# Optimization experiments

Hardware: AMD Instinct MI355X
Metric: run time of the kernel (lower is better)

The kernel has to match this reference:

```python
import jax, jax.numpy as jnp
import numpy as np

IN_F = 4096
OUT_F = 4096
M_PAD = 4096   # next pow2 >= OUT_F
N_PAD = 4096   # next pow2 >= IN_F
CB_SIZE = 256  # E8 codebook entries, each an 8-dim vector


def fht(x):
    """Normalized fast Hadamard transform along the last axis (power-of-2 length)."""
    n = x.shape[-1]
    lead = x.shape[:-1]
    x = x.reshape(-1, n)
    h = 1
    while h < n:  # log2(n) static iterations -> jit-friendly
        x = x.reshape(-1, n // (2 * h), 2, h)
        a, b = x[:, :, 0, :], x[:, :, 1, :]
        x = jnp.stack((a + b, a - b), axis=2).reshape(-1, n)
        h *= 2
    return (x * np.float32(1.0 / np.sqrt(n))).reshape(*lead, n)


def setup_inputs() -> dict:
    key = jax.random.key(0)
    k_x, k_q, k_su, k_sv, k_cb = jax.random.split(key, 5)
    x = jax.random.normal(k_x, (4, 2048, IN_F), dtype=jnp.float32)
    Qidxs = jax.random.randint(k_q, (M_PAD, N_PAD // 8), 0, CB_SIZE, dtype=jnp.int32)
    # sign vectors are +-1 (random Hadamard transform signs)
    SU = jnp.where(jax.random.normal(k_su, (M_PAD,)) >= 0, 1.0, -1.0).astype(jnp.float32)
    SV = jnp.where(jax.random.normal(k_sv, (N_PAD,)) >= 0, 1.0, -1.0).astype(jnp.float32)
    Wscale = jnp.ones((), dtype=jnp.float32)
    codebook = jax.random.normal(k_cb, (CB_SIZE, 8), dtype=jnp.float32)
    return {"x": x, "Qidxs": Qidxs, "SU": SU, "SV": SV, "Wscale": Wscale, "codebook": codebook}


def reference(x, Qidxs, SU, SV, Wscale, codebook):
    shape = x.shape
    xf = x.reshape(-1, IN_F).astype(jnp.float32)          # (B, in)
    x_pad = jnp.pad(xf, ((0, 0), (0, N_PAD - IN_F)))      # (B, n_pad)
    # 1) input -> RHT domain: sign flip then Hadamard
    x_rht = fht(x_pad * SV[None, :])
    # 2) decode codebook indices into dense RHT-domain weight (m_pad, n_pad)
    W_rht = codebook[Qidxs.reshape(-1)].reshape(M_PAD, N_PAD)
    # 3) GEMM in RHT domain with global scale
    y_rht = (x_rht @ W_rht.T) * Wscale
    # 4) output RHT inverse: Hadamard then sign flip, unpad
    y = fht(y_rht) * SU[None, :]
    y = y[:, :OUT_F]
    return y.reshape(*shape[:-1], OUT_F)
```

## Files before the change

### kernel.cpp

```cpp
#include <hip/hip_runtime.h>
#include <hip/hip_bf16.h>


using short8 = __attribute__((ext_vector_type(8))) short;
using f32x4  = __attribute__((ext_vector_type(4))) float;

#define AS1 __attribute__((address_space(1)))
#define AS3 __attribute__((address_space(3)))

__device__ __forceinline__ unsigned short f2bf(float f) {
  unsigned int u = __float_as_uint(f);
  unsigned int r = (u + 0x7fffu + ((u >> 16) & 1u)) >> 16;
  return (unsigned short)r;
}

__device__ __forceinline__ void gload16(const void* g, void* l) {
  __builtin_amdgcn_global_load_lds((const AS1 void*)g, (AS3 void*)l, 16, 0, 0);
}

#define WAIT_VM4 asm volatile("s_waitcnt vmcnt(4)" ::: "memory")
#define WAIT_VM0 asm volatile("s_waitcnt vmcnt(0)" ::: "memory")
#define LGKM0    asm volatile("s_waitcnt lgkmcnt(0)" ::: "memory")
#define SB       __builtin_amdgcn_sched_barrier(0)
#define BAR      __builtin_amdgcn_s_barrier()
#define PRIO1    __builtin_amdgcn_s_setprio(1)
#define PRIO0    __builtin_amdgcn_s_setprio(0)

__global__ __launch_bounds__(256) void rht_in_kernel(const float* __restrict__ X,
                                                     const float* __restrict__ SV,
                                                     unsigned short* __restrict__ A) {
  __shared__ float tmp[4096];
  const int row = blockIdx.x;
  const int t = threadIdx.x;
  const size_t base = (size_t)row * 4096;
  float v[16];
#pragma unroll
  for (int j = 0; j < 16; ++j) {
    int c = j * 256 + t;
    v[j] = X[base + c] * SV[c];
  }
#pragma unroll
  for (int d = 1; d < 16; d <<= 1) {
#pragma unroll
    for (int j = 0; j < 16; ++j) {
      if ((j & d) == 0) {
        float a = v[j], b = v[j | d];
        v[j] = a + b;
        v[j | d] = a - b;
      }
    }
  }
  const int lane = t & 63;
#pragma unroll
  for (int d = 1; d < 64; d <<= 1) {
#pragma unroll
    for (int j = 0; j < 16; ++j) {
      float p = __shfl_xor(v[j], d, 64);
      v[j] = (lane & d) ? (p - v[j]) : (v[j] + p);
    }
  }
#pragma unroll
  for (int dd = 0; dd < 2; ++dd) {
    const int d = 64 << dd;
    if (dd) __syncthreads();
#pragma unroll
    for (int j = 0; j < 16; ++j) tmp[j * 256 + t] = v[j];
    __syncthreads();
#pragma unroll
    for (int j = 0; j < 16; ++j) {
      float p = tmp[j * 256 + (t ^ d)];
      v[j] = (t & d) ? (p - v[j]) : (v[j] + p);
    }
  }
#pragma unroll
  for (int j = 0; j < 16; ++j) A[base + j * 256 + t] = f2bf(v[j]);
}

__global__ __launch_bounds__(256) void decode_w_kernel(const int* __restrict__ Q,
                                                       const float* __restrict__ cb,
                                                       unsigned short* __restrict__ W) {
  const int e = blockIdx.x * 256 + threadIdx.x;
  const int idx = Q[e];
  const float4* c = (const float4*)(cb + (size_t)idx * 8);
  float4 c0 = c[0], c1 = c[1];
  union { short8 v; unsigned short u[8]; } w;
  w.u[0] = f2bf(c0.x); w.u[1] = f2bf(c0.y); w.u[2] = f2bf(c0.z); w.u[3] = f2bf(c0.w);
  w.u[4] = f2bf(c1.x); w.u[5] = f2bf(c1.y); w.u[6] = f2bf(c1.z); w.u[7] = f2bf(c1.w);
  *(short8*)&W[(size_t)e * 8] = w.v;
}

#define MFMA1(mi, ni, av, bv) \
  acc[mi][ni] = __builtin_amdgcn_mfma_f32_16x16x32_bf16(av, bv, acc[mi][ni], 0, 0, 0)

#define MFMA16(MB, a0_, a1_, a2_, a3_, bx0, bx1, bx2, bx3) do {           \
  MFMA1(MB + 0, 0, a0_, bx0); MFMA1(MB + 0, 1, a0_, bx1);                 \
  MFMA1(MB + 0, 2, a0_, bx2); MFMA1(MB + 0, 3, a0_, bx3);                 \
  MFMA1(MB + 1, 0, a1_, bx0); MFMA1(MB + 1, 1, a1_, bx1);                 \
  MFMA1(MB + 1, 2, a1_, bx2); MFMA1(MB + 1, 3, a1_, bx3);                 \
  MFMA1(MB + 2, 0, a2_, bx0); MFMA1(MB + 2, 1, a2_, bx1);                 \
  MFMA1(MB + 2, 2, a2_, bx2); MFMA1(MB + 2, 3, a2_, bx3);                 \
  MFMA1(MB + 3, 0, a3_, bx0); MFMA1(MB + 3, 1, a3_, bx1);                 \
  MFMA1(MB + 3, 2, a3_, bx2); MFMA1(MB + 3, 3, a3_, bx3);                 \
} while (0)

#define RD_A4(r0, r1, r2, r3, BC, KS, MB) do {                            \
  r0 = *(const short8*)&sA[BC][KS][wm + (MB + 0) * 16 + fr][qc];          \
  r1 = *(const short8*)&sA[BC][KS][wm + (MB + 1) * 16 + fr][qc];          \
  r2 = *(const short8*)&sA[BC][KS][wm + (MB + 2) * 16 + fr][qc];          \
  r3 = *(const short8*)&sA[BC][KS][wm + (MB + 3) * 16 + fr][qc];          \
} while (0)

#define RD_B4(r0, r1, r2, r3, BC, KS) do {                                \
  r0 = *(const short8*)&sB[BC][KS][wn + 0 * 16 + fr][qc];                 \
  r1 = *(const short8*)&sB[BC][KS][wn + 1 * 16 + fr][qc];                 \
  r2 = *(const short8*)&sB[BC][KS][wn + 2 * 16 + fr][qc];                 \
  r3 = *(const short8*)&sB[BC][KS][wn + 3 * 16 + fr][qc];                 \
} while (0)

#define STAGE_A(BB, H, KTN) do {                                          \
  const unsigned short* gp_ = Ag + (KTN) * 64 + (H) * 32;                 \
  gload16(gp_, (unsigned short*)&sA[BB][H][0][0] + d0);                   \
  gload16(gp_ + (size_t)128 * 4096, (unsigned short*)&sA[BB][H][0][0] + d1); \
} while (0)

#define STAGE_B(BB, H, KTN) do {                                          \
  const unsigned short* gp_ = Bg + (KTN) * 64 + (H) * 32;                 \
  gload16(gp_, (unsigned short*)&sB[BB][H][0][0] + d0);                   \
  gload16(gp_ + (size_t)128 * 4096, (unsigned short*)&sB[BB][H][0][0] + d1); \
} while (0)

#define TILE(BC, BN_, KTN, DS, LASTF) do {                                \
           \
  RD_A4(aS0_0, aS0_1, aS0_2, aS0_3, BC, 0, 0);                            \
  RD_B4(bA_0, bA_1, bA_2, bA_3, BC, 0);                                   \
  if (DS) { STAGE_A(BN_, 0, KTN); }                                       \
  BAR; LGKM0; SB;                                                         \
  RD_A4(aS1_0, aS1_1, aS1_2, aS1_3, BC, 0, 4); SB;                        \
  PRIO1; MFMA16(0, aS0_0, aS0_1, aS0_2, aS0_3, bA_0, bA_1, bA_2, bA_3);   \
  PRIO0; BAR;                                                             \
                 \
  if (DS) { STAGE_B(BN_, 0, KTN); }                                       \
  BAR; LGKM0; SB;                                                         \
  if (LASTF) { WAIT_VM0; } else { WAIT_VM4; }                             \
  RD_A4(aS0_0, aS0_1, aS0_2, aS0_3, BC, 1, 0);                            \
  RD_B4(bB_0, bB_1, bB_2, bB_3, BC, 1); SB;                               \
  PRIO1; MFMA16(4, aS1_0, aS1_1, aS1_2, aS1_3, bA_0, bA_1, bA_2, bA_3);   \
  PRIO0; BAR;                                                             \
                                     \
  if (DS) { STAGE_A(BN_, 1, KTN); }                                       \
  BAR; LGKM0; SB;                                                         \
  RD_A4(aS1_0, aS1_1, aS1_2, aS1_3, BC, 1, 4); SB;                        \
  PRIO1; MFMA16(0, aS0_0, aS0_1, aS0_2, aS0_3, bB_0, bB_1, bB_2, bB_3);   \
  PRIO0; BAR;                                                             \
            \
  if (DS) { STAGE_B(BN_, 1, KTN); }                                       \
  BAR; LGKM0; SB;                                                         \
  PRIO1; MFMA16(4, aS1_0, aS1_1, aS1_2, aS1_3, bB_0, bB_1, bB_2, bB_3);   \
  PRIO0;                                                                  \
  if (!(LASTF)) { WAIT_VM4; }                                             \
  BAR;                                                                    \
} while (0)

__global__ __launch_bounds__(512, 2) void gemm_bt_kernel(const unsigned short* __restrict__ A,
                                                         const unsigned short* __restrict__ B,
                                                         float* __restrict__ C) {
  __shared__ unsigned short sA[2][2][256][32];
  __shared__ unsigned short sB[2][2][256][32];

  const int bid = blockIdx.x;
  const int swz = (bid & 7) * 64 + (bid >> 3);
  const int tm = swz >> 4;
  const int tn = swz & 15;

  const int t = threadIdx.x;
  const int lane = t & 63;
  const int w = t >> 6;
  const int wm = (w >> 2) * 128;
  const int wn = (w & 3) * 64;
  const int fr = lane & 15;
  const int qc = ((lane >> 4) ^ ((lane >> 1) & 3)) * 8;

  const int sr = t >> 2;
  const int sc = ((t & 3) ^ ((t >> 3) & 3)) * 8;
  const unsigned short* Ag = A + (size_t)(tm * 256 + sr) * 4096 + sc;
  const unsigned short* Bg = B + (size_t)(tn * 256 + sr) * 4096 + sc;
  const int d0 = t * 8;
  const int d1 = (512 + t) * 8;

  f32x4 acc[8][4];
#pragma unroll
  for (int m = 0; m < 8; ++m)
#pragma unroll
    for (int n = 0; n < 4; ++n) {
      f32x4 z = {0.f, 0.f, 0.f, 0.f};
      acc[m][n] = z;
    }
  short8 aS0_0, aS0_1, aS0_2, aS0_3;
  short8 aS1_0, aS1_1, aS1_2, aS1_3;
  short8 bA_0, bA_1, bA_2, bA_3;
  short8 bB_0, bB_1, bB_2, bB_3;

  STAGE_A(0, 0, 0); STAGE_B(0, 0, 0); STAGE_A(0, 1, 0); STAGE_B(0, 1, 0);
  WAIT_VM4;
  BAR;

  for (int k2 = 0; k2 < 31; ++k2) {
    TILE(0, 1, 2 * k2 + 1, 1, 0);
    TILE(1, 0, 2 * k2 + 2, 1, 0);
  }
  TILE(0, 1, 63, 1, 0);
  TILE(1, 0, 64, 0, 1);

  const size_t crow0 = (size_t)tm * 256 + wm + (lane >> 4) * 4;
  const int ccol0 = tn * 256 + wn + fr;
#pragma unroll
  for (int mf = 0; mf < 8; ++mf)
#pragma unroll
    for (int j = 0; j < 4; ++j) {
      float* Cp = C + (crow0 + mf * 16 + j) * 4096 + ccol0;
#pragma unroll
      for (int nf = 0; nf < 4; ++nf) Cp[nf * 16] = acc[mf][nf][j];
    }
}

__global__ __launch_bounds__(256) void rht_out_kernel(float* __restrict__ Y,
                                                      const float* __restrict__ SU,
                                                      const float* __restrict__ Wscale) {
  __shared__ float tmp[4096];
  const int row = blockIdx.x;
  const int t = threadIdx.x;
  const size_t base = (size_t)row * 4096;
  float v[16];
#pragma unroll
  for (int j = 0; j < 16; ++j) v[j] = Y[base + j * 256 + t];
#pragma unroll
  for (int d = 1; d < 16; d <<= 1) {
#pragma unroll
    for (int j = 0; j < 16; ++j) {
      if ((j & d) == 0) {
        float a = v[j], b = v[j | d];
        v[j] = a + b;
        v[j | d] = a - b;
      }
    }
  }
  const int lane = t & 63;
#pragma unroll
  for (int d = 1; d < 64; d <<= 1) {
#pragma unroll
    for (int j = 0; j < 16; ++j) {
      float p = __shfl_xor(v[j], d, 64);
      v[j] = (lane & d) ? (p - v[j]) : (v[j] + p);
    }
  }
#pragma unroll
  for (int dd = 0; dd < 2; ++dd) {
    const int d = 64 << dd;
    if (dd) __syncthreads();
#pragma unroll
    for (int j = 0; j < 16; ++j) tmp[j * 256 + t] = v[j];
    __syncthreads();
#pragma unroll
    for (int j = 0; j < 16; ++j) {
      float p = tmp[j * 256 + (t ^ d)];
      v[j] = (t & d) ? (p - v[j]) : (v[j] + p);
    }
  }
  const float ws = Wscale[0] * (1.0f / 4096.0f);
#pragma unroll
  for (int j = 0; j < 16; ++j) {
    int c = j * 256 + t;
    Y[base + c] = v[j] * SU[c] * ws;
  }
}

extern "C" void kernel_launch(void* const* d_in, const int* in_sizes, int n_in,
                              void* d_out, int out_size, void* d_ws, size_t ws_size,
                              hipStream_t stream) {
  const float* x      = (const float*)d_in[0];
  const int*   Qidxs  = (const int*)d_in[1];
  const float* SU     = (const float*)d_in[2];
  const float* SV     = (const float*)d_in[3];
  const float* Wscale = (const float*)d_in[4];
  const float* cb     = (const float*)d_in[5];
  float* out = (float*)d_out;

  unsigned short* Arht = (unsigned short*)d_ws;
  unsigned short* W    = (unsigned short*)((char*)d_ws + (size_t)8192 * 4096 * 2);

  rht_in_kernel<<<8192, 256, 0, stream>>>(x, SV, Arht);
  decode_w_kernel<<<(4096 * 512) / 256, 256, 0, stream>>>(Qidxs, cb, W);
  gemm_bt_kernel<<<512, 512, 0, stream>>>(Arht, W, out);
  rht_out_kernel<<<8192, 256, 0, stream>>>(out, SU, Wscale);
}
```

Measured before the change: 356.3 us.

## Fold both Hadamard transforms into the decoded weight matrix

Because the Hadamard transforms are linear, they are applied to the 4096x4096 weight instead of to the 8192-row activations and outputs: W' = diag(SU)·H·W·H. The weight is decoded and row-transformed in one kernel, then column-transformed in two passes over bf16 intermediates. The GEMM then writes the final output directly, which removes the FHT over the input and output activations. The cost is extra bf16 rounding of the transformed weight at each pass, plus three weight passes over 4096x4096, with strided loads in the column passes.

```diff
diff --git a/kernel.cpp b/kernel.cpp
--- a/kernel.cpp
+++ b/kernel.cpp
@@ -12,6 +12,10 @@
   unsigned int u = __float_as_uint(f);
   unsigned int r = (u + 0x7fffu + ((u >> 16) & 1u)) >> 16;
   return (unsigned short)r;
+}
+
+__device__ __forceinline__ float bf2f(unsigned short u) {
+  return __uint_as_float((unsigned int)u << 16);
 }
 
 __device__ __forceinline__ void gload16(const void* g, void* l) {
@@ -26,37 +30,67 @@
 #define PRIO1    __builtin_amdgcn_s_setprio(1)
 #define PRIO0    __builtin_amdgcn_s_setprio(0)
 
-__global__ __launch_bounds__(256) void rht_in_kernel(const float* __restrict__ X,
-                                                     const float* __restrict__ SV,
-                                                     unsigned short* __restrict__ A) {
+#define H16_REGS(v)                                                       \
+  _Pragma("unroll")                                                       \
+  for (int d = 1; d < 16; d <<= 1) {                                      \
+    _Pragma("unroll")                                                     \
+    for (int j = 0; j < 16; ++j) {                                        \
+      if ((j & d) == 0) {                                                 \
+        float a_ = v[j], b_ = v[j | d];                                   \
+        v[j] = a_ + b_;                                                   \
+        v[j | d] = a_ - b_;                                               \
+      }                                                                   \
+    }                                                                     \
+  }
+
+__global__ __launch_bounds__(256) void zconv_kernel(const float* __restrict__ X,
+                                                    const float* __restrict__ SV,
+                                                    unsigned short* __restrict__ Z) {
+  const size_t idx = ((size_t)blockIdx.x * 256 + threadIdx.x) * 16;
+  const int c0 = (int)(idx & 4095);
+  const float4* X4 = (const float4*)(X + idx);
+  const float4* SV4 = (const float4*)(SV + c0);
+  union { short8 s; unsigned short u[8]; } lo, hi;
+#pragma unroll
+  for (int q = 0; q < 2; ++q) {
+    float4 a = X4[2 * q], b = X4[2 * q + 1];
+    float4 sa = SV4[2 * q], sb = SV4[2 * q + 1];
+    unsigned short* o = q ? hi.u : lo.u;
+    o[0] = f2bf(a.x * sa.x); o[1] = f2bf(a.y * sa.y);
+    o[2] = f2bf(a.z * sa.z); o[3] = f2bf(a.w * sa.w);
+    o[4] = f2bf(b.x * sb.x); o[5] = f2bf(b.y * sb.y);
+    o[6] = f2bf(b.z * sb.z); o[7] = f2bf(b.w * sb.w);
+  }
+  short8* Zp = (short8*)(Z + idx);
+  Zp[0] = lo.s;
+  Zp[1] = hi.s;
+}
+
+__global__ __launch_bounds__(256) void decode_rowfht_kernel(const int* __restrict__ Q,
+                                                            const float* __restrict__ cb,
+                                                            unsigned short* __restrict__ Wa) {
   __shared__ float tmp[4096];
   const int row = blockIdx.x;
   const int t = threadIdx.x;
-  const size_t base = (size_t)row * 4096;
+  const int lane = t & 63;
   float v[16];
-#pragma unroll
-  for (int j = 0; j < 16; ++j) {
-    int c = j * 256 + t;
-    v[j] = X[base + c] * SV[c];
-  }
-#pragma unroll
-  for (int d = 1; d < 16; d <<= 1) {
-#pragma unroll
-    for (int j = 0; j < 16; ++j) {
-      if ((j & d) == 0) {
-        float a = v[j], b = v[j | d];
-        v[j] = a + b;
-        v[j | d] = a - b;
-      }
-    }
-  }
-  const int lane = t & 63;
+  int2 qi = *(const int2*)&Q[(size_t)row * 512 + 2 * t];
+  {
+    const float4* c0 = (const float4*)(cb + (size_t)qi.x * 8);
+    const float4* c1 = (const float4*)(cb + (size_t)qi.y * 8);
+    float4 p0 = c0[0], p1 = c0[1], p2 = c1[0], p3 = c1[1];
+    v[0] = p0.x;  v[1] = p0.y;  v[2] = p0.z;  v[3] = p0.w;
+    v[4] = p1.x;  v[5] = p1.y;  v[6] = p1.z;  v[7] = p1.w;
+    v[8] = p2.x;  v[9] = p2.y;  v[10] = p2.z; v[11] = p2.w;
+    v[12] = p3.x; v[13] = p3.y; v[14] = p3.z; v[15] = p3.w;
+  }
+  H16_REGS(v)
 #pragma unroll
   for (int d = 1; d < 64; d <<= 1) {
 #pragma unroll
     for (int j = 0; j < 16; ++j) {
-      float p = __shfl_xor(v[j], d, 64);
-      v[j] = (lane & d) ? (p - v[j]) : (v[j] + p);
+      float p_ = __shfl_xor(v[j], d, 64);
+      v[j] = (lane & d) ? (p_ - v[j]) : (v[j] + p_);
     }
   }
 #pragma unroll
@@ -68,25 +102,69 @@
     __syncthreads();
 #pragma unroll
     for (int j = 0; j < 16; ++j) {
-      float p = tmp[j * 256 + (t ^ d)];
-      v[j] = (t & d) ? (p - v[j]) : (v[j] + p);
-    }
-  }
-#pragma unroll
-  for (int j = 0; j < 16; ++j) A[base + j * 256 + t] = f2bf(v[j]);
-}
-
-__global__ __launch_bounds__(256) void decode_w_kernel(const int* __restrict__ Q,
-                                                       const float* __restrict__ cb,
-                                                       unsigned short* __restrict__ W) {
-  const int e = blockIdx.x * 256 + threadIdx.x;
-  const int idx = Q[e];
-  const float4* c = (const float4*)(cb + (size_t)idx * 8);
-  float4 c0 = c[0], c1 = c[1];
-  union { short8 v; unsigned short u[8]; } w;
-  w.u[0] = f2bf(c0.x); w.u[1] = f2bf(c0.y); w.u[2] = f2bf(c0.z); w.u[3] = f2bf(c0.w);
-  w.u[4] = f2bf(c1.x); w.u[5] = f2bf(c1.y); w.u[6] = f2bf(c1.z); w.u[7] = f2bf(c1.w);
-  *(short8*)&W[(size_t)e * 8] = w.v;
+      float p_ = tmp[j * 256 + (t ^ d)];
+      v[j] = (t & d) ? (p_ - v[j]) : (v[j] + p_);
+    }
+  }
+  union { short8 s; unsigned short u[8]; } lo, hi;
+#pragma unroll
+  for (int j = 0; j < 8; ++j) {
+    lo.u[j] = f2bf(v[j] * (1.0f / 64.0f));
+    hi.u[j] = f2bf(v[8 + j] * (1.0f / 64.0f));
+  }
+  short8* Wp = (short8*)(Wa + (size_t)row * 4096 + t * 16);
+  Wp[0] = lo.s;
+  Wp[1] = hi.s;
+}
+
+template <int PASS>
+__global__ __launch_bounds__(256) void fht_wcol_kernel(const unsigned short* __restrict__ Win,
+                                                       unsigned short* __restrict__ Wout,
+                                                       const float* __restrict__ SU,
+                                                       const float* __restrict__ Wscale) {
+  __shared__ float tmp[64 * 64];
+  const int rg = blockIdx.x >> 6;
+  const int cg = blockIdx.x & 63;
+  const int t = threadIdx.x;
+  const int cl = t & 63;
+  const int q = t >> 6;
+  const int c = cg * 64 + cl;
+  float v[16];
+#pragma unroll
+  for (int j = 0; j < 16; ++j) {
+    const int rloc = q * 16 + j;
+    const int row = (PASS == 0) ? (rg * 64 + rloc) : (rloc * 64 + rg);
+    v[j] = bf2f(Win[(size_t)row * 4096 + c]);
+  }
+  H16_REGS(v)
+#pragma unroll
+  for (int dd = 0; dd < 2; ++dd) {
+    const int d = 16 << dd;
+    if (dd) __syncthreads();
+#pragma unroll
+    for (int j = 0; j < 16; ++j) tmp[(q * 16 + j) * 64 + cl] = v[j];
+    __syncthreads();
+#pragma unroll
+    for (int j = 0; j < 16; ++j) {
+      const int rloc = q * 16 + j;
+      float p_ = tmp[(rloc ^ d) * 64 + cl];
+      v[j] = (rloc & d) ? (p_ - v[j]) : (v[j] + p_);
+    }
+  }
+  if (PASS == 0) {
+#pragma unroll
+    for (int j = 0; j < 16; ++j) {
+      const int row = rg * 64 + q * 16 + j;
+      Wout[(size_t)row * 4096 + c] = f2bf(v[j] * 0.125f);
+    }
+  } else {
+    const float ws = Wscale[0] * 0.125f;
+#pragma unroll
+    for (int j = 0; j < 16; ++j) {
+      const int row = (q * 16 + j) * 64 + rg;
+      Wout[(size_t)row * 4096 + c] = f2bf(v[j] * SU[row] * ws);
+    }
+  }
 }
 
 #define MFMA1(mi, ni, av, bv) \
@@ -223,57 +301,6 @@
     }
 }
 
-__global__ __launch_bounds__(256) void rht_out_kernel(float* __restrict__ Y,
-                                                      const float* __restrict__ SU,
-                                                      const float* __restrict__ Wscale) {
-  __shared__ float tmp[4096];
-  const int row = blockIdx.x;
-  const int t = threadIdx.x;
-  const size_t base = (size_t)row * 4096;
-  float v[16];
-#pragma unroll
-  for (int j = 0; j < 16; ++j) v[j] = Y[base + j * 256 + t];
-#pragma unroll
-  for (int d = 1; d < 16; d <<= 1) {
-#pragma unroll
-    for (int j = 0; j < 16; ++j) {
-      if ((j & d) == 0) {
-        float a = v[j], b = v[j | d];
-        v[j] = a + b;
-        v[j | d] = a - b;
-      }
-    }
-  }
-  const int lane = t & 63;
-#pragma unroll
-  for (int d = 1; d < 64; d <<= 1) {
-#pragma unroll
-    for (int j = 0; j < 16; ++j) {
-      float p = __shfl_xor(v[j], d, 64);
-      v[j] = (lane & d) ? (p - v[j]) : (v[j] + p);
-    }
-  }
-#pragma unroll
-  for (int dd = 0; dd < 2; ++dd) {
-    const int d = 64 << dd;
-    if (dd) __syncthreads();
-#pragma unroll
-    for (int j = 0; j < 16; ++j) tmp[j * 256 + t] = v[j];
-    __syncthreads();
-#pragma unroll
-    for (int j = 0; j < 16; ++j) {
-      float p = tmp[j * 256 + (t ^ d)];
-      v[j] = (t & d) ? (p - v[j]) : (v[j] + p);
-    }
-  }
-  const float ws = Wscale[0] * (1.0f / 4096.0f);
-#pragma unroll
-  for (int j = 0; j < 16; ++j) {
-    int c = j * 256 + t;
-    Y[base + c] = v[j] * SU[c] * ws;
-  }
-}
-
 extern "C" void kernel_launch(void* const* d_in, const int* in_sizes, int n_in,
                               void* d_out, int out_size, void* d_ws, size_t ws_size,
                               hipStream_t stream) {
@@ -285,11 +312,13 @@
   const float* cb     = (const float*)d_in[5];
   float* out = (float*)d_out;
 
-  unsigned short* Arht = (unsigned short*)d_ws;
-  unsigned short* W    = (unsigned short*)((char*)d_ws + (size_t)8192 * 4096 * 2);
-
-  rht_in_kernel<<<8192, 256, 0, stream>>>(x, SV, Arht);
-  decode_w_kernel<<<(4096 * 512) / 256, 256, 0, stream>>>(Qidxs, cb, W);
-  gemm_bt_kernel<<<512, 512, 0, stream>>>(Arht, W, out);
-  rht_out_kernel<<<8192, 256, 0, stream>>>(out, SU, Wscale);
-}
+  unsigned short* Z  = (unsigned short*)d_ws;
+  unsigned short* Wa = (unsigned short*)((char*)d_ws + (size_t)64 * 1024 * 1024);
+  unsigned short* Wb = (unsigned short*)((char*)d_ws + (size_t)96 * 1024 * 1024);
+
+  zconv_kernel<<<8192, 256, 0, stream>>>(x, SV, Z);
+  decode_rowfht_kernel<<<4096, 256, 0, stream>>>(Qidxs, cb, Wa);
+  fht_wcol_kernel<0><<<4096, 256, 0, stream>>>(Wa, Wb, SU, Wscale);
+  fht_wcol_kernel<1><<<4096, 256, 0, stream>>>(Wb, Wa, SU, Wscale);
+  gemm_bt_kernel<<<512, 512, 0, stream>>>(Z, Wa, out);
+}
```

New measurement: 353.2 us. About the same (-0.9%).
